# Kernel optimization log

Measured on AMD Instinct MI355X. Metric: run time of the kernel, lower is better.

The kernel has to match this reference:

```python
import jax, jax.numpy as jnp
import numpy as np

N_MENTIONS = 4096
N_PAIRS = 32768
N_SEGMENTS = 1024  # number of spans (ragged softmax groups)
G_DIM = 3 * 768    # span representation dim (3*embed_dim)
D_IN = 3 * G_DIM + 20
HIDDEN = 150


def setup_inputs() -> dict:
    key = jax.random.key(0)
    ks = jax.random.split(key, 11)
    inp = {
        "g_i": jax.random.normal(ks[0], (N_MENTIONS, G_DIM), jnp.float32),
        "mention_scores": jax.random.normal(ks[1], (N_MENTIONS, 1), jnp.float32),
        "speaker_embed": jax.random.normal(ks[2], (3, 20), jnp.float32) * 0.02,
        "W1": jax.random.normal(ks[3], (D_IN, HIDDEN), jnp.float32) * (1.0 / np.sqrt(D_IN)),
        "b1": jnp.zeros((HIDDEN,), jnp.float32),
        "W2": jax.random.normal(ks[4], (HIDDEN, 1), jnp.float32) * (1.0 / np.sqrt(HIDDEN)),
        "b2": jnp.zeros((1,), jnp.float32),
        "mention_ids": jax.random.randint(ks[5], (N_PAIRS,), 0, N_MENTIONS),
        "antecedent_ids": jax.random.randint(ks[6], (N_PAIRS,), 0, N_MENTIONS),
        "speaker_labels": jax.random.randint(ks[7], (N_PAIRS,), 0, 3),
        "segment_ids": jnp.sort(jax.random.randint(ks[8], (N_PAIRS,), 0, N_SEGMENTS)),
    }
    return inp


def reference(g_i, mention_scores, speaker_embed, W1, b1, W2, b2,
              mention_ids, antecedent_ids, speaker_labels, segment_ids):
    # Gather mention / antecedent span representations. [P, G]
    i_g = g_i[mention_ids]
    j_g = g_i[antecedent_ids]
    phi = speaker_embed[speaker_labels]  # [P, speaker_dim]

    # Pair features: cat(i_g, j_g, i_g*j_g, phi). [P, D_IN]
    pairs = jnp.concatenate([i_g, j_g, i_g * j_g, phi], axis=1)

    # Score MLP: Linear -> ReLU -> Linear(->1). (dropout off in eval)
    h = jax.nn.relu(pairs @ W1 + b1)          # [P, HIDDEN]
    s_ij = (h @ W2 + b2)[:, 0]                # [P]

    # coref score = s_i + s_j + s_ij
    s_i = mention_scores[mention_ids, 0]
    s_j = mention_scores[antecedent_ids, 0]
    scores = s_i + s_j + s_ij                 # [P]

    # Ragged per-span softmax with an appended epsilon logit of 0.0.
    seg_max = jax.ops.segment_max(scores, segment_ids, num_segments=N_SEGMENTS)
    m = jnp.maximum(seg_max, 0.0)             # include epsilon=0 in the max
    e = jnp.exp(scores - m[segment_ids])      # [P]
    eps_e = jnp.exp(-m)                       # [S] exp(0 - m)
    denom = jax.ops.segment_sum(e, segment_ids, num_segments=N_SEGMENTS) + eps_e
    pair_probs = e / denom[segment_ids]       # [P]
    eps_probs = eps_e / denom                 # [S]

    # Flattened: all pair probs followed by the per-span epsilon probs.
    return jnp.concatenate([pair_probs, eps_probs])
```

## Files before the change

### kernel.cpp

```cpp
#include <hip/hip_runtime.h>
#include <cstdint>

#define NM   4096
#define NP   32768
#define NSEG 1024
#define GD   2304
#define HID  150
#define NPAD 160
#define KG32 72
#define SEG_ELEMS (KG32 * 10 * 512)

typedef unsigned short u16;
typedef short s16x8 __attribute__((ext_vector_type(8)));
typedef float f32x4 __attribute__((ext_vector_type(4)));
typedef uint32_t u32x4 __attribute__((ext_vector_type(4)));

union Frag {
    uint32_t u[4];
    s16x8    v;
};

__device__ inline uint32_t cvtpk(float lo, float hi) {
    uint32_t r;
    asm("v_cvt_pk_bf16_f32 %0, %1, %2" : "=v"(r) : "v"(lo), "v"(hi));
    return r;
}

__device__ inline f32x4 mfma16(s16x8 a, s16x8 b, f32x4 c) {
    return __builtin_amdgcn_mfma_f32_16x16x32_bf16(a, b, c, 0, 0, 0);
}

__device__ inline s16x8 prodpack(u32x4 iu, u32x4 ju) {
    Frag f;
#pragma unroll
    for (int m = 0; m < 4; ++m) {
        uint32_t x = iu[m], y = ju[m];
        float lo = __builtin_bit_cast(float, x << 16) *
                   __builtin_bit_cast(float, y << 16);
        float hi = __builtin_bit_cast(float, x & 0xffff0000u) *
                   __builtin_bit_cast(float, y & 0xffff0000u);
        f.u[m] = cvtpk(lo, hi);
    }
    return f.v;
}

__global__ void prep_pack_kernel(const float* __restrict__ W1,
                                 u16* __restrict__ wpack) {
    int idx = blockIdx.x * 256 + threadIdx.x;
    if (idx >= 3 * KG32 * 10 * 64) return;
    int lane = idx & 63;
    int t    = idx >> 6;
    int nf   = t % 10;
    int sk   = t / 10;
    int seg  = sk / KG32, kg = sk % KG32;
    int kbase = (seg == 0) ? 2 * GD : ((seg == 1) ? 0 : GD);
    int n    = nf * 16 + (lane & 15);
    int krow = kbase + kg * 32 + ((lane >> 4) << 3);
    u32x4 d = (u32x4){0u, 0u, 0u, 0u};
    if (n < HID) {
#pragma unroll
        for (int jj = 0; jj < 4; ++jj) {
            float v0 = W1[(size_t)(krow + 2 * jj) * HID + n];
            float v1 = W1[(size_t)(krow + 2 * jj + 1) * HID + n];
            d[jj] = cvtpk(v0, v1);
        }
    }
    *(u32x4*)(wpack + (size_t)idx * 8) = d;
}

__global__ void prep_tables_kernel(const float* __restrict__ spk,
                                   const float* __restrict__ W1,
                                   const float* __restrict__ b1,
                                   const float* __restrict__ W2,
                                   float* __restrict__ phib,
                                   float* __restrict__ w2pad) {
    int t = threadIdx.x;
    if (t < 3 * NPAD) {
        int s = t / NPAD, n = t - s * NPAD;
        float a = 0.f;
        if (n < HID) {
            for (int d = 0; d < 20; ++d)
                a = fmaf(spk[s * 20 + d], W1[(size_t)(3 * GD + d) * HID + n], a);
            a += b1[n];
        }
        phib[t] = a;
    } else if (t < 4 * NPAD) {
        int n = t - 3 * NPAD;
        w2pad[n] = (n < HID) ? W2[n] : 0.f;
    }
}

struct A2 { f32x4 x0, x1; };

__launch_bounds__(256)
__global__ void gemm_pre_kernel(const float* __restrict__ gi,
                                const u16* __restrict__ wpackIJ,
                                u16* __restrict__ gbf,
                                float* __restrict__ APre) {
    const int tid = threadIdx.x;
    const int kh = tid >> 6, lane = tid & 63;
    const int quad = lane >> 4, l15 = lane & 15;
    const int mt = blockIdx.x, ng = blockIdx.y;
    const u16* wp = wpackIJ + (size_t)ng * SEG_ELEMS + lane * 8;
    const int row = mt * 16 + l15;

    __shared__ float xch[3][64][44];

    f32x4 acc[10];
#pragma unroll
    for (int b = 0; b < 10; ++b) acc[b] = (f32x4){0.f, 0.f, 0.f, 0.f};

    const float* ap = gi + (size_t)row * GD + quad * 8;
    u16* gb = gbf + (size_t)row * GD + quad * 8;
    const bool emit = (ng == 0);
    const int u0 = kh * 18;

    A2 a0, a1, a2;
    Frag b0[10], b1[10];

#define LDA(ax, k) { ax.x0 = *(const f32x4*)(ap + (u0 + (k)) * 32); \
                     ax.x1 = *(const f32x4*)(ap + (u0 + (k)) * 32 + 4); }
#define LDBP(bb, k) { const u16* wn = wp + (size_t)(u0 + (k)) * 5120; \
        _Pragma("unroll") for (int nf = 0; nf < 10; ++nf) \
            bb[nf].v = *(const s16x8*)(const void*)(wn + nf * 512); }
#define PHP(k, ax, bb) { \
        Frag a; \
        a.u[0] = cvtpk(ax.x0[0], ax.x0[1]); a.u[1] = cvtpk(ax.x0[2], ax.x0[3]); \
        a.u[2] = cvtpk(ax.x1[0], ax.x1[1]); a.u[3] = cvtpk(ax.x1[2], ax.x1[3]); \
        if (emit) *(u32x4*)(gb + (u0 + (k)) * 32) = *(const u32x4*)a.u; \
        __builtin_amdgcn_s_setprio(1); \
        _Pragma("unroll") for (int nf = 0; nf < 10; ++nf) \
            acc[nf] = mfma16(a.v, bb[nf].v, acc[nf]); \
        __builtin_amdgcn_s_setprio(0); }

    LDBP(b0, 0); LDBP(b1, 1);
    LDA(a0, 0); LDA(a1, 1); LDA(a2, 2);

#pragma unroll 1
    for (int t = 0; t < 2; ++t) {
        const int kb = t * 6;
        PHP(kb + 0, a0, b0); LDBP(b0, kb + 2); LDA(a0, kb + 3);
        PHP(kb + 1, a1, b1); LDBP(b1, kb + 3); LDA(a1, kb + 4);
        PHP(kb + 2, a2, b0); LDBP(b0, kb + 4); LDA(a2, kb + 5);
        PHP(kb + 3, a0, b1); LDBP(b1, kb + 5); LDA(a0, kb + 6);
        PHP(kb + 4, a1, b0); LDBP(b0, kb + 6); LDA(a1, kb + 7);
        PHP(kb + 5, a2, b1); LDBP(b1, kb + 7); LDA(a2, kb + 8);
    }
    PHP(12, a0, b0); LDBP(b0, 14); LDA(a0, 15);
    PHP(13, a1, b1); LDBP(b1, 15); LDA(a1, 16);
    PHP(14, a2, b0); LDBP(b0, 16); LDA(a2, 17);
    PHP(15, a0, b1); LDBP(b1, 17);
    PHP(16, a1, b0);
    PHP(17, a2, b1);

#undef LDA
#undef LDBP
#undef PHP

    if (kh != 0) {
        float* dst = &xch[kh - 1][lane][0];
#pragma unroll
        for (int nf = 0; nf < 10; ++nf)
            *(f32x4*)(dst + nf * 4) = acc[nf];
    }
    __syncthreads();
    if (kh == 0) {
#pragma unroll
        for (int k = 0; k < 3; ++k) {
            const float* src = &xch[k][lane][0];
#pragma unroll
            for (int nf = 0; nf < 10; ++nf)
                acc[nf] += *(const f32x4*)(src + nf * 4);
        }
        const int colbase = ng * NPAD + l15;
        float* Ap = APre + (size_t)(mt * 16 + quad * 4) * 320 + colbase;
#pragma unroll
        for (int nf = 0; nf < 10; ++nf)
#pragma unroll
            for (int r = 0; r < 4; ++r)
                Ap[(size_t)r * 320 + nf * 16] = acc[nf][r];
    }
}

struct G4 { u32x4 i0, j0, i1, j1; };

__launch_bounds__(128)
__global__ void gemm_pairs_kernel(const u16* __restrict__ gbf,
                                  const u16* __restrict__ wpackP,
                                  const float* __restrict__ APre,
                                  const float* __restrict__ phib,
                                  const float* __restrict__ w2pad,
                                  const float* __restrict__ mscore,
                                  const float* __restrict__ b2,
                                  const int* __restrict__ mids,
                                  const int* __restrict__ aids,
                                  const int* __restrict__ slab,
                                  float* __restrict__ scores) {
    const int tid = threadIdx.x;
    const int wave = tid >> 6, lane = tid & 63;
    const int quad = lane >> 4, l15 = lane & 15;
    const int base = blockIdx.x * 64 + wave * 32;

    f32x4 acc[2][10];
#pragma unroll
    for (int a = 0; a < 2; ++a)
#pragma unroll
        for (int b = 0; b < 10; ++b) acc[a][b] = (f32x4){0.f, 0.f, 0.f, 0.f};

    const int p0 = base + l15, p1 = base + 16 + l15;
    const u16* ip0 = gbf + (size_t)mids[p0] * GD + quad * 8;
    const u16* jp0 = gbf + (size_t)aids[p0] * GD + quad * 8;
    const u16* ip1 = gbf + (size_t)mids[p1] * GD + quad * 8;
    const u16* jp1 = gbf + (size_t)aids[p1] * GD + quad * 8;
    const u16* wl = wpackP + lane * 8;

    G4 g0, g1, g2, g3;
    Frag b0[10], b1[10];

#define LDG(g, k) { const int off = (k) * 32; \
        g.i0 = *(const u32x4*)(ip0 + off); g.j0 = *(const u32x4*)(jp0 + off); \
        g.i1 = *(const u32x4*)(ip1 + off); g.j1 = *(const u32x4*)(jp1 + off); }
#define LDB(bb, k) { const u16* wn = wl + (size_t)(k) * 5120; \
        _Pragma("unroll") for (int nf = 0; nf < 10; ++nf) \
            bb[nf].v = *(const s16x8*)(const void*)(wn + nf * 512); }
#define PH(g, bb) { \
        s16x8 a0 = prodpack(g.i0, g.j0); \
        s16x8 a1 = prodpack(g.i1, g.j1); \
        __builtin_amdgcn_s_setprio(1); \
        _Pragma("unroll") for (int nf = 0; nf < 10; ++nf) { \
            acc[0][nf] = mfma16(a0, bb[nf].v, acc[0][nf]); \
            acc[1][nf] = mfma16(a1, bb[nf].v, acc[1][nf]); } \
        __builtin_amdgcn_s_setprio(0); }

    LDB(b0, 0); LDB(b1, 1);
    LDG(g0, 0); LDG(g1, 1); LDG(g2, 2); LDG(g3, 3);

#pragma unroll 1
    for (int t = 0; t < 17; ++t) {
        const int kb = t * 4;
        PH(g0, b0); LDB(b0, kb + 2); LDG(g0, kb + 4);
        PH(g1, b1); LDB(b1, kb + 3); LDG(g1, kb + 5);
        PH(g2, b0); LDB(b0, kb + 4); LDG(g2, kb + 6);
        PH(g3, b1); LDB(b1, kb + 5); LDG(g3, kb + 7);
    }
    PH(g0, b0); LDB(b0, 70);
    PH(g1, b1); LDB(b1, 71);
    PH(g2, b0);
    PH(g3, b1);

#undef LDG
#undef LDB
#undef PH

    float w2v[10];
#pragma unroll
    for (int nf = 0; nf < 10; ++nf) w2v[nf] = w2pad[nf * 16 + l15];
    const float b2v = b2[0];

#pragma unroll
    for (int mf = 0; mf < 2; ++mf)
#pragma unroll
        for (int r = 0; r < 4; ++r) {
            const int p  = base + mf * 16 + quad * 4 + r;
            const int mi = mids[p], ai = aids[p], sp = slab[p];
            const float* Ai = APre + (size_t)mi * 320;
            const float* Bj = APre + (size_t)ai * 320 + NPAD;
            const float* Ph = phib + sp * NPAD;
            float partial = 0.f;
#pragma unroll
            for (int nf = 0; nf < 10; ++nf) {
                const int c = nf * 16 + l15;
                float h = acc[mf][nf][r] + Ai[c] + Bj[c] + Ph[c];
                h = fmaxf(h, 0.f);
                partial = fmaf(h, w2v[nf], partial);
            }
            partial += __shfl_xor(partial, 1);
            partial += __shfl_xor(partial, 2);
            partial += __shfl_xor(partial, 4);
            partial += __shfl_xor(partial, 8);
            if (l15 == 0)
                scores[p] = partial + b2v + mscore[mi] + mscore[ai];
        }
}

__global__ void seg_softmax_kernel(const float* __restrict__ scores,
                                   const int* __restrict__ seg,
                                   float* __restrict__ out) {
    const int s = blockIdx.x;
    const int lane = threadIdx.x;
    int lo = 0, hi = NP;
    while (lo < hi) { int mid = (lo + hi) >> 1; if (seg[mid] < s) lo = mid + 1; else hi = mid; }
    const int start = lo;
    int lo2 = start, hi2 = NP;
    while (lo2 < hi2) { int mid = (lo2 + hi2) >> 1; if (seg[mid] <= s) lo2 = mid + 1; else hi2 = mid; }
    const int end = lo2;

    float m = 0.f;
    for (int i = start + lane; i < end; i += 64) m = fmaxf(m, scores[i]);
#pragma unroll
    for (int msk = 1; msk < 64; msk <<= 1) m = fmaxf(m, __shfl_xor(m, msk));

    float sum = 0.f;
    for (int i = start + lane; i < end; i += 64) sum += __expf(scores[i] - m);
#pragma unroll
    for (int msk = 1; msk < 64; msk <<= 1) sum += __shfl_xor(sum, msk);

    const float epse = __expf(-m);
    const float inv  = 1.f / (sum + epse);
    for (int i = start + lane; i < end; i += 64) out[i] = __expf(scores[i] - m) * inv;
    if (lane == 0) out[NP + s] = epse * inv;
}

extern "C" void kernel_launch(void* const* d_in, const int* in_sizes, int n_in,
                              void* d_out, int out_size, void* d_ws, size_t ws_size,
                              hipStream_t stream) {
    const float* gi     = (const float*)d_in[0];
    const float* mscore = (const float*)d_in[1];
    const float* spk    = (const float*)d_in[2];
    const float* W1     = (const float*)d_in[3];
    const float* b1     = (const float*)d_in[4];
    const float* W2     = (const float*)d_in[5];
    const float* b2     = (const float*)d_in[6];
    const int*   mids   = (const int*)d_in[7];
    const int*   aids   = (const int*)d_in[8];
    const int*   slab   = (const int*)d_in[9];
    const int*   segs   = (const int*)d_in[10];
    float* out = (float*)d_out;

    char* w = (char*)d_ws;
    u16*   gbf    = (u16*)w;
    u16*   wpack  = (u16*)(w + 18874368);
    float* APre   = (float*)(w + 21086208);
    float* scores = (float*)(w + 26329088);
    float* phib   = (float*)(w + 26460160);
    float* w2pad  = (float*)(w + 26462080);

    prep_pack_kernel<<<dim3((3 * KG32 * 10 * 64 + 255) / 256), dim3(256), 0, stream>>>(W1, wpack);
    prep_tables_kernel<<<dim3(1), dim3(640), 0, stream>>>(spk, W1, b1, W2, phib, w2pad);
    gemm_pre_kernel<<<dim3(256, 2), dim3(256), 0, stream>>>(gi, wpack + SEG_ELEMS, gbf, APre);
    gemm_pairs_kernel<<<dim3(512), dim3(128), 0, stream>>>(gbf, wpack, APre, phib, w2pad,
                                                           mscore, b2, mids, aids, slab, scores);
    seg_softmax_kernel<<<dim3(NSEG), dim3(64), 0, stream>>>(scores, segs, out);
}
```

Measured before the change: 193.1 us.

## Sort pairs by mention id to improve gather locality in pair GEMM

Adds a single-block counting sort that builds a permutation of pairs grouped by mention id, merged into the table-prep kernel. The pair GEMM processes pairs in permuted order so rows of the bf16 span table are reused across nearby tiles, and it still writes scores back to their original positions. The pair-kernel pipeline is also reworked from four gather buffers to three with a 6-step unroll, and the s_setprio hints are removed from both GEMMs. This trades an extra serial single-block sort and an indirection load for better L2 reuse, though the j-side gathers stay random.

```diff
diff --git a/kernel.cpp b/kernel.cpp
--- a/kernel.cpp
+++ b/kernel.cpp
@@ -68,13 +68,21 @@
     *(u32x4*)(wpack + (size_t)idx * 8) = d;
 }
 
-__global__ void prep_tables_kernel(const float* __restrict__ spk,
-                                   const float* __restrict__ W1,
-                                   const float* __restrict__ b1,
-                                   const float* __restrict__ W2,
-                                   float* __restrict__ phib,
-                                   float* __restrict__ w2pad) {
-    int t = threadIdx.x;
+__global__ __launch_bounds__(1024)
+void prep_sort_kernel(const float* __restrict__ spk,
+                      const float* __restrict__ W1,
+                      const float* __restrict__ b1,
+                      const float* __restrict__ W2,
+                      const int* __restrict__ mids,
+                      float* __restrict__ phib,
+                      float* __restrict__ w2pad,
+                      int* __restrict__ perm) {
+    __shared__ int cnt[NM];
+    __shared__ int bas[NM];
+    __shared__ int lsum[1024];
+
+    const int t = threadIdx.x;
+
     if (t < 3 * NPAD) {
         int s = t / NPAD, n = t - s * NPAD;
         float a = 0.f;
@@ -88,6 +96,42 @@
         int n = t - 3 * NPAD;
         w2pad[n] = (n < HID) ? W2[n] : 0.f;
     }
+
+#pragma unroll
+    for (int j = 0; j < 4; ++j) cnt[t + j * 1024] = 0;
+    __syncthreads();
+
+    for (int p = t; p < NP; p += 1024) atomicAdd(&cnt[mids[p]], 1);
+    __syncthreads();
+
+    int v[4];
+    int s = 0;
+#pragma unroll
+    for (int j = 0; j < 4; ++j) { v[j] = cnt[4 * t + j]; s += v[j]; }
+    int val = s;
+    lsum[t] = val;
+    __syncthreads();
+    for (int off = 1; off < 1024; off <<= 1) {
+        int x = (t >= off) ? lsum[t - off] : 0;
+        __syncthreads();
+        val += x;
+        lsum[t] = val;
+        __syncthreads();
+    }
+    int run = val - s;
+#pragma unroll
+    for (int j = 0; j < 4; ++j) {
+        bas[4 * t + j] = run;
+        run += v[j];
+        cnt[4 * t + j] = 0;
+    }
+    __syncthreads();
+
+    for (int p = t; p < NP; p += 1024) {
+        int m = mids[p];
+        int pos = bas[m] + atomicAdd(&cnt[m], 1);
+        perm[pos] = p;
+    }
 }
 
 struct A2 { f32x4 x0, x1; };
@@ -128,10 +172,8 @@
         a.u[0] = cvtpk(ax.x0[0], ax.x0[1]); a.u[1] = cvtpk(ax.x0[2], ax.x0[3]); \
         a.u[2] = cvtpk(ax.x1[0], ax.x1[1]); a.u[3] = cvtpk(ax.x1[2], ax.x1[3]); \
         if (emit) *(u32x4*)(gb + (u0 + (k)) * 32) = *(const u32x4*)a.u; \
-        __builtin_amdgcn_s_setprio(1); \
         _Pragma("unroll") for (int nf = 0; nf < 10; ++nf) \
-            acc[nf] = mfma16(a.v, bb[nf].v, acc[nf]); \
-        __builtin_amdgcn_s_setprio(0); }
+            acc[nf] = mfma16(a.v, bb[nf].v, acc[nf]); }
 
     LDBP(b0, 0); LDBP(b1, 1);
     LDA(a0, 0); LDA(a1, 1); LDA(a2, 2);
@@ -195,6 +237,7 @@
                                   const int* __restrict__ mids,
                                   const int* __restrict__ aids,
                                   const int* __restrict__ slab,
+                                  const int* __restrict__ perm,
                                   float* __restrict__ scores) {
     const int tid = threadIdx.x;
     const int wave = tid >> 6, lane = tid & 63;
@@ -207,14 +250,14 @@
 #pragma unroll
         for (int b = 0; b < 10; ++b) acc[a][b] = (f32x4){0.f, 0.f, 0.f, 0.f};
 
-    const int p0 = base + l15, p1 = base + 16 + l15;
+    const int p0 = perm[base + l15], p1 = perm[base + 16 + l15];
     const u16* ip0 = gbf + (size_t)mids[p0] * GD + quad * 8;
     const u16* jp0 = gbf + (size_t)aids[p0] * GD + quad * 8;
     const u16* ip1 = gbf + (size_t)mids[p1] * GD + quad * 8;
     const u16* jp1 = gbf + (size_t)aids[p1] * GD + quad * 8;
     const u16* wl = wpackP + lane * 8;
 
-    G4 g0, g1, g2, g3;
+    G4 g0, g1, g2;
     Frag b0[10], b1[10];
 
 #define LDG(g, k) { const int off = (k) * 32; \
@@ -226,27 +269,29 @@
 #define PH(g, bb) { \
         s16x8 a0 = prodpack(g.i0, g.j0); \
         s16x8 a1 = prodpack(g.i1, g.j1); \
-        __builtin_amdgcn_s_setprio(1); \
         _Pragma("unroll") for (int nf = 0; nf < 10; ++nf) { \
             acc[0][nf] = mfma16(a0, bb[nf].v, acc[0][nf]); \
-            acc[1][nf] = mfma16(a1, bb[nf].v, acc[1][nf]); } \
-        __builtin_amdgcn_s_setprio(0); }
-
+            acc[1][nf] = mfma16(a1, bb[nf].v, acc[1][nf]); } }
+
+    LDG(g0, 0); LDG(g1, 1); LDG(g2, 2);
     LDB(b0, 0); LDB(b1, 1);
-    LDG(g0, 0); LDG(g1, 1); LDG(g2, 2); LDG(g3, 3);
 
 #pragma unroll 1
-    for (int t = 0; t < 17; ++t) {
-        const int kb = t * 4;
-        PH(g0, b0); LDB(b0, kb + 2); LDG(g0, kb + 4);
-        PH(g1, b1); LDB(b1, kb + 3); LDG(g1, kb + 5);
-        PH(g2, b0); LDB(b0, kb + 4); LDG(g2, kb + 6);
-        PH(g3, b1); LDB(b1, kb + 5); LDG(g3, kb + 7);
-    }
-    PH(g0, b0); LDB(b0, 70);
-    PH(g1, b1); LDB(b1, 71);
-    PH(g2, b0);
-    PH(g3, b1);
+    for (int t = 0; t < 11; ++t) {
+        const int kb = t * 6;
+        PH(g0, b0); LDG(g0, kb + 3); LDB(b0, kb + 2);
+        PH(g1, b1); LDG(g1, kb + 4); LDB(b1, kb + 3);
+        PH(g2, b0); LDG(g2, kb + 5); LDB(b0, kb + 4);
+        PH(g0, b1); LDG(g0, kb + 6); LDB(b1, kb + 5);
+        PH(g1, b0); LDG(g1, kb + 7); LDB(b0, kb + 6);
+        PH(g2, b1); LDG(g2, kb + 8); LDB(b1, kb + 7);
+    }
+    PH(g0, b0); LDG(g0, 69); LDB(b0, 68);
+    PH(g1, b1); LDG(g1, 70); LDB(b1, 69);
+    PH(g2, b0); LDG(g2, 71); LDB(b0, 70);
+    PH(g0, b1); LDB(b1, 71);
+    PH(g1, b0);
+    PH(g2, b1);
 
 #undef LDG
 #undef LDB
@@ -261,7 +306,7 @@
     for (int mf = 0; mf < 2; ++mf)
 #pragma unroll
         for (int r = 0; r < 4; ++r) {
-            const int p  = base + mf * 16 + quad * 4 + r;
+            const int p  = perm[base + mf * 16 + quad * 4 + r];
             const int mi = mids[p], ai = aids[p], sp = slab[p];
             const float* Ai = APre + (size_t)mi * 320;
             const float* Bj = APre + (size_t)ai * 320 + NPAD;
@@ -334,11 +379,14 @@
     float* scores = (float*)(w + 26329088);
     float* phib   = (float*)(w + 26460160);
     float* w2pad  = (float*)(w + 26462080);
+    int*   perm   = (int*)(w + 26462720);
 
     prep_pack_kernel<<<dim3((3 * KG32 * 10 * 64 + 255) / 256), dim3(256), 0, stream>>>(W1, wpack);
-    prep_tables_kernel<<<dim3(1), dim3(640), 0, stream>>>(spk, W1, b1, W2, phib, w2pad);
+    prep_sort_kernel<<<dim3(1), dim3(1024), 0, stream>>>(spk, W1, b1, W2, mids,
+                                                         phib, w2pad, perm);
     gemm_pre_kernel<<<dim3(256, 2), dim3(256), 0, stream>>>(gi, wpack + SEG_ELEMS, gbf, APre);
     gemm_pairs_kernel<<<dim3(512), dim3(128), 0, stream>>>(gbf, wpack, APre, phib, w2pad,
-                                                           mscore, b2, mids, aids, slab, scores);
+                                                           mscore, b2, mids, aids, slab,
+                                                           perm, scores);
     seg_softmax_kernel<<<dim3(NSEG), dim3(64), 0, stream>>>(scores, segs, out);
 }
```

Result: slower. 224.8 us (+16.4%).
